# Kernel optimization log

Hardware: AMD Instinct MI355X
Metric: run time of the kernel (lower is better)

Reference implementation:

```python
import jax, jax.numpy as jnp
import numpy as np

NUM_HEADS = 8
BLOCK = 8      # block_size
HALO = 2       # kernel_size (halo width)


def _rel_to_abs(rel):
    # halo-style relative->absolute conversion
    # rel: [B, G, qh, qw, 2*p-1] -> [B, G, qh, qw, p]
    B, G, qh, qw, dim = rel.shape
    p = (dim + 1) // 2
    gap = p - qw
    flat = rel.reshape(B, G, qh, qw * dim)[:, :, :, qw - 1:-1]
    return flat.reshape(B, G, qh, qw, 2 * (p - 1))[:, :, :, :, gap:p + gap]


def _relative_logits(pos_q, pos_emb_h, pos_emb_w):
    # pos_q: [B, G, qb, qb, kd]; pos_emb_*: [kd, 2*p-1]
    rel_w = _rel_to_abs(jnp.einsum('bghwd,dr->bghwr', pos_q, pos_emb_w))  # [B,G,qb,qb,p] key-width
    q_t = pos_q.transpose(0, 1, 3, 2, 4)
    rel_h = _rel_to_abs(jnp.einsum('bgwhd,dr->bgwhr', q_t, pos_emb_h))
    rel_h = rel_h.transpose(0, 1, 3, 2, 4)  # [B,G,qb,qb,p] key-height
    return rel_h[..., :, None] + rel_w[..., None, :]  # [B,G,qb,qb,p,p]


def reference(x, w_q, w_kv, w_out, pos_emb_h, pos_emb_w):
    B, H, W, C = x.shape
    kd = C // NUM_HEADS                # per-head key dim
    kvk = BLOCK + 2 * HALO             # halo window size
    out_ch = w_out.shape[1]
    v_dim = out_ch // NUM_HEADS
    kv_per_head = (C + out_ch) // NUM_HEADS
    hh, ww = H // BLOCK, W // BLOCK
    scale = float(1.0 / np.sqrt(kd))

    # ---- query (1x1 conv == matmul), blockify ----
    q = (x @ w_q).reshape(B, hh, BLOCK, ww, BLOCK, NUM_HEADS, kd)
    q = q.transpose(0, 5, 1, 3, 2, 4, 6)  # [B,nh,hh,ww,qb,qb,kd]
    attn_q = q.reshape(B, NUM_HEADS, hh, ww, BLOCK * BLOCK, kd) * scale
    pos_q = q.reshape(B, NUM_HEADS * hh * ww, BLOCK, BLOCK, kd)

    # ---- key/value: 1x1 conv, halo pad, unfold into overlapping windows ----
    kv = jnp.pad(x @ w_kv, ((0, 0), (HALO, HALO), (HALO, HALO), (0, 0)))
    idx = np.arange(hh)[:, None] * BLOCK + np.arange(kvk)[None, :]  # [hh,kvk]
    idy = np.arange(ww)[:, None] * BLOCK + np.arange(kvk)[None, :]  # [ww,kvk]
    patches = kv[:, idx][:, :, :, idy]           # [B,hh,kvk,ww,kvk,kv_dim]
    patches = patches.transpose(0, 1, 3, 2, 4, 5)  # [B,hh,ww,kvk,kvk,kv_dim]
    kvh = patches.reshape(B, hh, ww, kvk, kvk, NUM_HEADS, kv_per_head)
    kvh = kvh.transpose(0, 5, 1, 2, 3, 4, 6).reshape(B, NUM_HEADS, hh, ww, kvk * kvk, kv_per_head)
    key, value = kvh[..., :kd], kvh[..., kd:]

    # ---- attention with relative position bias ----
    scores = jnp.einsum('bnhwqd,bnhwkd->bnhwqk', attn_q, key)
    pos = _relative_logits(pos_q, pos_emb_h, pos_emb_w)
    pos = pos.reshape(B, NUM_HEADS, hh, ww, BLOCK * BLOCK, kvk * kvk)
    attn = jax.nn.softmax(scores + pos, axis=-1)
    out = jnp.einsum('bnhwqk,bnhwkv->bnhwqv', attn, value)  # [B,nh,hh,ww,qb*qb,v_dim]

    # ---- de-blockify, output projection ----
    out = out.reshape(B, NUM_HEADS, hh, ww, BLOCK, BLOCK, v_dim)
    out = out.transpose(0, 2, 4, 3, 5, 1, 6).reshape(B, H, W, NUM_HEADS * v_dim)
    return out @ w_out


def setup_inputs() -> dict:
    key = jax.random.key(0)
    ks = jax.random.split(key, 6)
    B, H, W, C = 4, 128, 128, 256
    out_ch = 256
    kd = C // NUM_HEADS
    kvk = BLOCK + 2 * HALO
    std = kd ** -0.5
    return {
        'x': jax.random.normal(ks[0], (B, H, W, C), jnp.float32),
        'w_q': jax.random.normal(ks[1], (C, C), jnp.float32) * 0.02,
        'w_kv': jax.random.normal(ks[2], (C, C + out_ch), jnp.float32) * 0.02,
        'w_out': jax.random.normal(ks[3], (C, out_ch), jnp.float32) * 0.02,
        'pos_emb_h': jax.random.normal(ks[4], (kd, 2 * kvk - 1), jnp.float32) * std,
        'pos_emb_w': jax.random.normal(ks[5], (kd, 2 * kvk - 1), jnp.float32) * std,
    }
```

## Files before the change

kernel.cpp:

```cpp
#include <hip/hip_runtime.h>
#include <hip/hip_bf16.h>
#include <cstdint>


#define KVK 12
#define NKEYS 144
#define VT_S 160
#define PT_S 168
#define LOG2E 1.4426950408889634f

typedef unsigned int u32;
typedef unsigned long long u64;
typedef unsigned short u16;
typedef __attribute__((ext_vector_type(8))) __bf16 bf16x8;
typedef __attribute__((ext_vector_type(4))) float f32x4;

__device__ __forceinline__ u16 f2bf(float f) {
    u32 x = __float_as_uint(f);
    return (u16)((x + 0x7fffu + ((x >> 16) & 1u)) >> 16);
}
__device__ __forceinline__ u32 cvtpk(float lo, float hi) {
    u32 d;
    asm("v_cvt_pk_bf16_f32 %0, %1, %2" : "=v"(d) : "v"(lo), "v"(hi));
    return d;
}
__device__ __forceinline__ float max3f(float a, float b, float c) {
    float d;
    asm("v_max3_f32 %0, %1, %2, %3" : "=v"(d) : "v"(a), "v"(b), "v"(c));
    return d;
}
__device__ __forceinline__ float exp2a(float x) {
    float d;
    asm("v_exp_f32 %0, %1" : "=v"(d) : "v"(x));
    return d;
}
__device__ __forceinline__ void gload16(const void* g, void* l) {
    __builtin_amdgcn_global_load_lds(
        (const __attribute__((address_space(1))) void*)g,
        (__attribute__((address_space(3))) void*)l, 16, 0, 0);
}
__device__ __forceinline__ u32 pack2(float lo, float hi) {
    return (u32)f2bf(lo) | ((u32)f2bf(hi) << 16);
}

__global__ __launch_bounds__(256) void conv_prep(const float* __restrict__ x,
                                                 u16* __restrict__ xb,
                                                 const float* __restrict__ wq,
                                                 const float* __restrict__ wkv,
                                                 const float* __restrict__ wout,
                                                 u16* __restrict__ wT,
                                                 u16* __restrict__ woutT,
                                                 const float* __restrict__ emb_h,
                                                 const float* __restrict__ emb_w,
                                                 u16* __restrict__ embT) {
    int blk = blockIdx.x, t = threadIdx.x;
    if (blk < 8192) {
        int i = blk * 256 + t;
        const float4* p = reinterpret_cast<const float4*>(x) + (long)i * 2;
        float4 a = p[0], b = p[1];
        uint4 o;
        o.x = pack2(a.x, a.y); o.y = pack2(a.z, a.w);
        o.z = pack2(b.x, b.y); o.w = pack2(b.z, b.w);
        reinterpret_cast<uint4*>(xb)[i] = o;
        return;
    }
    blk -= 8192;
    if (blk < 256) {
        int idx = blk * 256 + t; int nn = idx >> 8, k = idx & 255;
        wT[idx] = f2bf(wq[(long)k * 256 + nn]);
    } else if (blk < 768) {
        int idx = (blk - 256) * 256 + t; int nn = idx >> 8, k = idx & 255;
        float v = wkv[(long)k * 512 + nn];
        if ((nn & 32) == 0) v *= 0.2550348642f;
        wT[65536 + idx] = f2bf(v);
    } else if (blk < 1024) {
        int idx = (blk - 768) * 256 + t; int nn = idx >> 8, k = idx & 255;
        woutT[idx] = f2bf(wout[(long)k * 256 + nn]);
    } else if (blk == 1024) {
        for (int i = t; i < 1024; i += 256) {
            int p = i >> 5, d = i & 31;
            embT[i] = (p < 23) ? f2bf(emb_h[d * 23 + p]) : 0;
        }
    } else {
        for (int i = t; i < 1024; i += 256) {
            int p = i >> 5, d = i & 31;
            embT[1024 + i] = (p < 23) ? f2bf(emb_w[d * 23 + p]) : 0;
        }
    }
}

__global__ __launch_bounds__(256) void gemm_qkv6(const u16* __restrict__ A,
                                                 const u16* __restrict__ WT,
                                                 u16* __restrict__ Qb,
                                                 u16* __restrict__ KVb) {
    __shared__ u16 As[8192];
    __shared__ u16 Bs[8192];
    const int t = threadIdx.x;
    const int bid = blockIdx.x;
    const int mIdx = (bid / 48) * 8 + (bid & 7);
    const int nt = (bid >> 3) % 6;
    const int w = t >> 6, lane = t & 63;
    const long m0 = (long)mIdx * 128;
    const long n0 = (long)nt * 128;
    const int wr = w >> 1, wc = w & 1;
    const int r = lane & 15, g = lane >> 4;

    f32x4 acc[4][4];
    #pragma unroll
    for (int i = 0; i < 4; ++i)
        #pragma unroll
        for (int j = 0; j < 4; ++j) acc[i][j] = (f32x4){0.f, 0.f, 0.f, 0.f};

    const u16* Ags[4];
    const u16* Bgs[4];
    #pragma unroll
    for (int cq = 0; cq < 4; ++cq) {
        int u = cq * 256 + w * 64 + lane;
        int panel = u >> 9, row = (u >> 2) & 127, col8 = (u & 3) * 8;
        Ags[cq] = A + (m0 + row) * 256 + panel * 32 + col8;
        Bgs[cq] = WT + (n0 + row) * 256 + panel * 32 + col8;
    }

    for (int k0 = 0; k0 < 256; k0 += 64) {
        #pragma unroll
        for (int cq = 0; cq < 4; ++cq) {
            gload16(Ags[cq] + k0, &As[cq * 2048 + w * 512]);
            gload16(Bgs[cq] + k0, &Bs[cq * 2048 + w * 512]);
        }
        __syncthreads();
        #pragma unroll
        for (int kk = 0; kk < 2; ++kk) {
            bf16x8 a[4], b[4];
            #pragma unroll
            for (int i = 0; i < 4; ++i)
                a[i] = *reinterpret_cast<const bf16x8*>(
                    &As[kk * 4096 + (wr * 64 + i * 16 + r) * 32 + g * 8]);
            #pragma unroll
            for (int j = 0; j < 4; ++j)
                b[j] = *reinterpret_cast<const bf16x8*>(
                    &Bs[kk * 4096 + (wc * 64 + j * 16 + r) * 32 + g * 8]);
            #pragma unroll
            for (int i = 0; i < 4; ++i)
                #pragma unroll
                for (int j = 0; j < 4; ++j)
                    acc[i][j] = __builtin_amdgcn_mfma_f32_16x16x32_bf16(b[j], a[i], acc[i][j], 0, 0, 0);
        }
        __syncthreads();
    }

    const bool isQ = (nt < 2);
    #pragma unroll
    for (int i = 0; i < 4; ++i) {
        long row = m0 + wr * 64 + i * 16 + r;
        #pragma unroll
        for (int j = 0; j < 4; ++j) {
            long colb = n0 + wc * 64 + j * 16 + g * 4;
            uint2 st;
            st.x = cvtpk(acc[i][j][0], acc[i][j][1]);
            st.y = cvtpk(acc[i][j][2], acc[i][j][3]);
            if (isQ) *reinterpret_cast<uint2*>(Qb + row * 256 + colb) = st;
            else     *reinterpret_cast<uint2*>(KVb + row * 512 + colb - 256) = st;
        }
    }
}

__global__ __launch_bounds__(256) void mfma_gemm(const u16* __restrict__ A,
                                                 const u16* __restrict__ BT,
                                                 float* __restrict__ C, int N) {
    __shared__ u16 As[8192];
    __shared__ u16 Bs[8192];
    const int t = threadIdx.x;
    const int bid = blockIdx.x;
    const int mIdx = (bid / 16) * 8 + (bid & 7);
    const int nt = (bid >> 3) & 1;
    const int w = t >> 6, lane = t & 63;
    const long m0 = (long)mIdx * 128;
    const long n0 = (long)nt * 128;
    const int wr = w >> 1, wc = w & 1;
    const int r = lane & 15, g = lane >> 4;

    f32x4 acc[4][4];
    #pragma unroll
    for (int i = 0; i < 4; ++i)
        #pragma unroll
        for (int j = 0; j < 4; ++j) acc[i][j] = (f32x4){0.f, 0.f, 0.f, 0.f};

    const u16* Ags[4];
    const u16* Bgs[4];
    #pragma unroll
    for (int cq = 0; cq < 4; ++cq) {
        int u = cq * 256 + w * 64 + lane;
        int panel = u >> 9, row = (u >> 2) & 127, col8 = (u & 3) * 8;
        Ags[cq] = A + (m0 + row) * 256 + panel * 32 + col8;
        Bgs[cq] = BT + (n0 + row) * 256 + panel * 32 + col8;
    }

    for (int k0 = 0; k0 < 256; k0 += 64) {
        #pragma unroll
        for (int cq = 0; cq < 4; ++cq) {
            gload16(Ags[cq] + k0, &As[cq * 2048 + w * 512]);
            gload16(Bgs[cq] + k0, &Bs[cq * 2048 + w * 512]);
        }
        __syncthreads();
        #pragma unroll
        for (int kk = 0; kk < 2; ++kk) {
            bf16x8 a[4], b[4];
            #pragma unroll
            for (int i = 0; i < 4; ++i)
                a[i] = *reinterpret_cast<const bf16x8*>(
                    &As[kk * 4096 + (wr * 64 + i * 16 + r) * 32 + g * 8]);
            #pragma unroll
            for (int j = 0; j < 4; ++j)
                b[j] = *reinterpret_cast<const bf16x8*>(
                    &Bs[kk * 4096 + (wc * 64 + j * 16 + r) * 32 + g * 8]);
            #pragma unroll
            for (int i = 0; i < 4; ++i)
                #pragma unroll
                for (int j = 0; j < 4; ++j)
                    acc[i][j] = __builtin_amdgcn_mfma_f32_16x16x32_bf16(b[j], a[i], acc[i][j], 0, 0, 0);
        }
        __syncthreads();
    }

    #pragma unroll
    for (int i = 0; i < 4; ++i) {
        long row = m0 + wr * 64 + i * 16 + r;
        #pragma unroll
        for (int j = 0; j < 4; ++j) {
            long colb = n0 + wc * 64 + j * 16 + g * 4;
            float4 st = make_float4(acc[i][j][0], acc[i][j][1], acc[i][j][2], acc[i][j][3]);
            *reinterpret_cast<float4*>(C + row * N + colb) = st;
        }
    }
}

#define UNITLOAD(U, VK, VV, KD, VB) {                                          \
    int kk_ = (U) >> 2, p_ = (U) & 3;                                          \
    int ky_ = (kk_ * 171) >> 11, kx_ = kk_ - 12 * ky_;                         \
    int gy_ = by * 8 + ky_ - 2, gx_ = bx * 8 + kx_ - 2;                        \
    if (((unsigned)gy_ < 128u) && ((unsigned)gx_ < 128u)) {                    \
        const u16* bp_ = KVb + (((long)b * 128 + gy_) * 128 + gx_) * 512 + n * 64 + p_ * 8; \
        VK = *reinterpret_cast<const uint4*>(bp_);                             \
        VV = *reinterpret_cast<const uint4*>(bp_ + 32);                        \
    }                                                                          \
    KD = kk_ * 64 + ((p_ * 8) ^ ((kk_ & 7) << 3));                             \
    VB = (p_ * 8) * VT_S + (kk_ ^ (p_ << 3));                                  \
}
#define VSCAT(VV, VB) {                                                        \
    u16 tmp_[8];                                                               \
    *reinterpret_cast<uint4*>(tmp_) = VV;                                      \
    _Pragma("unroll")                                                          \
    for (int i_ = 0; i_ < 8; ++i_) Vt[(VB) + i_ * VT_S] = tmp_[i_];            \
}

__global__ __launch_bounds__(256, 5) void attn_mfma(const u16* __restrict__ Qb,
                                                    const u16* __restrict__ KVb,
                                                    const u16* __restrict__ embT,
                                                    u16* __restrict__ Ob) {
    __shared__ __align__(16) char blob[22528];
    u16* Ks  = (u16*)blob;
    u16* Qe  = (u16*)(blob + 18432);
    u16* PT  = (u16*)blob;
    __shared__ u16 Vt[32 * VT_S];

    const int gblk = blockIdx.x;
    const int n = gblk & 7;
    const int bx = (gblk >> 3) & 15;
    const int by = (gblk >> 7) & 15;
    const int b = gblk >> 11;
    const int t = threadIdx.x;
    const int w = t >> 6, lane = t & 63;
    const int g = lane >> 4, r = lane & 15;

    const int q = w * 16 + r;
    const int qi = q >> 3, qj = q & 7;
    const long qrow = ((long)b * 128 + by * 8 + qi) * 128 + bx * 8 + qj;

    bf16x8 qa1 = *reinterpret_cast<const bf16x8*>(Qb + qrow * 256 + n * 32 + g * 8);
    bf16x8 ah0 = *reinterpret_cast<const bf16x8*>(embT + r * 32 + g * 8);
    bf16x8 ah1 = *reinterpret_cast<const bf16x8*>(embT + (16 + r) * 32 + g * 8);
    bf16x8 aw0 = *reinterpret_cast<const bf16x8*>(embT + 1024 + r * 32 + g * 8);
    bf16x8 aw1 = *reinterpret_cast<const bf16x8*>(embT + 1024 + (16 + r) * 32 + g * 8);

    uint4 z4 = make_uint4(0u, 0u, 0u, 0u);
    uint4 vK0 = z4, vV0 = z4, vK1 = z4, vV1 = z4, vK2 = z4, vV2 = z4;
    int kd0 = 0, vb0 = 0, kd1 = 0, vb1 = 0, kd2 = 0, vb2 = 0;
    UNITLOAD(t, vK0, vV0, kd0, vb0);
    UNITLOAD(t + 256, vK1, vV1, kd1, vb1);
    if (t < 64) UNITLOAD(t + 512, vK2, vV2, kd2, vb2);

    for (int u = t; u < 576; u += 256) {
        int kk = u >> 2, uu = u & 3;
        int ky = (kk * 171) >> 11;
        int kx = kk - 12 * ky;
        int hy = ky - 8 * uu;
        int hx = 12 + kx - 8 * uu;
        u64 lo = 0, hi = 0;
        if ((unsigned)hy < 4u) lo |= 0x3F80ULL << (hy * 16);
        else if ((unsigned)hy < 8u) hi |= 0x3F80ULL << ((hy - 4) * 16);
        if ((unsigned)hx < 4u) lo |= 0x3F80ULL << (hx * 16);
        else if ((unsigned)hx < 8u) hi |= 0x3F80ULL << ((hx - 4) * 16);
        int col = (32 + uu * 8) ^ ((kk & 7) << 3);
        u64* dst = reinterpret_cast<u64*>(&Ks[kk * 64 + col]);
        dst[0] = lo;
        dst[1] = hi;
    }
    if (t < 64) *reinterpret_cast<uint4*>(&Qe[t * 32 + 24]) = z4;
    if (t >= 224) {
        int d = t - 224;
        int sw = ((d >> 3) & 3) << 3;
        *reinterpret_cast<uint4*>(&Vt[d * VT_S + (144 ^ sw)]) = z4;
        *reinterpret_cast<uint4*>(&Vt[d * VT_S + (152 ^ sw)]) = z4;
    }

    *reinterpret_cast<uint4*>(&Ks[kd0]) = vK0;
    *reinterpret_cast<uint4*>(&Ks[kd1]) = vK1;
    if (t < 64) *reinterpret_cast<uint4*>(&Ks[kd2]) = vK2;

    {
        f32x4 z = (f32x4){0.f, 0.f, 0.f, 0.f};
        __builtin_amdgcn_s_setprio(1);
        f32x4 rh0 = __builtin_amdgcn_mfma_f32_16x16x32_bf16(ah0, qa1, z, 0, 0, 0);
        f32x4 rh1 = __builtin_amdgcn_mfma_f32_16x16x32_bf16(ah1, qa1, z, 0, 0, 0);
        f32x4 rw0 = __builtin_amdgcn_mfma_f32_16x16x32_bf16(aw0, qa1, z, 0, 0, 0);
        f32x4 rw1 = __builtin_amdgcn_mfma_f32_16x16x32_bf16(aw1, qa1, z, 0, 0, 0);
        __builtin_amdgcn_s_setprio(0);
        #pragma unroll
        for (int ti = 0; ti < 2; ++ti) {
            #pragma unroll
            for (int e = 0; e < 4; ++e) {
                int p = ti * 16 + g * 4 + e;
                float vh = (ti ? rh1[e] : rh0[e]) * LOG2E;
                float vw = (ti ? rw1[e] : rw0[e]) * LOG2E;
                int kyd = p + qi - 11;
                int kxd = p + qj - 11;
                if ((unsigned)kyd < 12u) Qe[q * 32 + kyd] = f2bf(vh);
                if ((unsigned)kxd < 12u) Qe[q * 32 + 12 + kxd] = f2bf(vw);
            }
        }
    }

    VSCAT(vV0, vb0);
    VSCAT(vV1, vb1);
    if (t < 64) VSCAT(vV2, vb2);

    __syncthreads();

    bf16x8 qa2 = *reinterpret_cast<const bf16x8*>(&Qe[q * 32 + g * 8]);
    f32x4 acc[9];
    __builtin_amdgcn_s_setprio(1);
    #pragma unroll
    for (int j = 0; j < 9; ++j) {
        int krow = j * 16 + r;
        int sw = (r & 7) << 3;
        bf16x8 kb0 = *reinterpret_cast<const bf16x8*>(&Ks[krow * 64 + ((g * 8) ^ sw)]);
        bf16x8 kb1 = *reinterpret_cast<const bf16x8*>(&Ks[krow * 64 + ((32 + g * 8) ^ sw)]);
        f32x4 z = (f32x4){0.f, 0.f, 0.f, 0.f};
        acc[j] = __builtin_amdgcn_mfma_f32_16x16x32_bf16(kb1, qa2,
                 __builtin_amdgcn_mfma_f32_16x16x32_bf16(kb0, qa1, z, 0, 0, 0), 0, 0, 0);
    }
    __builtin_amdgcn_s_setprio(0);

    float mx = max3f(acc[0][0], acc[0][1], acc[0][2]);
    mx = fmaxf(mx, acc[0][3]);
    #pragma unroll
    for (int j = 1; j < 9; ++j)
        mx = max3f(mx, max3f(acc[j][0], acc[j][1], acc[j][2]), acc[j][3]);
    mx = fmaxf(mx, __shfl_xor(mx, 16));
    mx = fmaxf(mx, __shfl_xor(mx, 32));
    float s0 = 0.f, s1 = 0.f, s2 = 0.f, s3 = 0.f;
    u32 pkA[9], pkB[9];
    #pragma unroll
    for (int j = 0; j < 9; ++j) {
        float e0 = exp2a(acc[j][0] - mx);
        float e1 = exp2a(acc[j][1] - mx);
        float e2 = exp2a(acc[j][2] - mx);
        float e3 = exp2a(acc[j][3] - mx);
        s0 += e0; s1 += e1; s2 += e2; s3 += e3;
        pkA[j] = cvtpk(e0, e1);
        pkB[j] = cvtpk(e2, e3);
    }
    float sum = (s0 + s1) + (s2 + s3);
    sum += __shfl_xor(sum, 16);
    sum += __shfl_xor(sum, 32);
    const float inv = __builtin_amdgcn_rcpf(sum);

    __syncthreads();

    {
        const int ptb = q * PT_S;
        #pragma unroll
        for (int j = 0; j < 9; ++j)
            *reinterpret_cast<uint2*>(&PT[ptb + 16 * j + 4 * g]) = make_uint2(pkA[j], pkB[j]);
        if (g == 0) {
            *reinterpret_cast<uint4*>(&PT[ptb + 144]) = make_uint4(0u, 0u, 0u, 0u);
            *reinterpret_cast<uint4*>(&PT[ptb + 152]) = make_uint4(0u, 0u, 0u, 0u);
        }
    }

    const int sw0 = (r >> 3) << 3;
    const int sw1 = (2 + (r >> 3)) << 3;
    f32x4 o0 = (f32x4){0.f, 0.f, 0.f, 0.f};
    f32x4 o1 = (f32x4){0.f, 0.f, 0.f, 0.f};
    __builtin_amdgcn_s_setprio(1);
    #pragma unroll
    for (int kk = 0; kk < 5; ++kk) {
        bf16x8 pb = *reinterpret_cast<const bf16x8*>(&PT[q * PT_S + kk * 32 + g * 8]);
        bf16x8 va0 = *reinterpret_cast<const bf16x8*>(&Vt[r * VT_S + ((kk * 32 + g * 8) ^ sw0)]);
        bf16x8 va1 = *reinterpret_cast<const bf16x8*>(&Vt[(16 + r) * VT_S + ((kk * 32 + g * 8) ^ sw1)]);
        o0 = __builtin_amdgcn_mfma_f32_16x16x32_bf16(va0, pb, o0, 0, 0, 0);
        o1 = __builtin_amdgcn_mfma_f32_16x16x32_bf16(va1, pb, o1, 0, 0, 0);
    }
    __builtin_amdgcn_s_setprio(0);
    {
        uint2 st0, st1;
        st0.x = cvtpk(o0[0] * inv, o0[1] * inv);
        st0.y = cvtpk(o0[2] * inv, o0[3] * inv);
        st1.x = cvtpk(o1[0] * inv, o1[1] * inv);
        st1.y = cvtpk(o1[2] * inv, o1[3] * inv);
        *reinterpret_cast<uint2*>(Ob + qrow * 256 + n * 32 + g * 4) = st0;
        *reinterpret_cast<uint2*>(Ob + qrow * 256 + n * 32 + 16 + g * 4) = st1;
    }
}

extern "C" void kernel_launch(void* const* d_in, const int* in_sizes, int n_in,
                              void* d_out, int out_size, void* d_ws, size_t ws_size,
                              hipStream_t stream) {
    const float* x     = (const float*)d_in[0];
    const float* w_q   = (const float*)d_in[1];
    const float* w_kv  = (const float*)d_in[2];
    const float* w_out = (const float*)d_in[3];
    const float* emb_h = (const float*)d_in[4];
    const float* emb_w = (const float*)d_in[5];

    u16* xb = (u16*)d_out;
    u16* Qb = (u16*)((char*)d_out + (size_t)33554432);
    char* ws = (char*)d_ws;
    u16* KVb   = (u16*)(ws);
    u16* Ob    = (u16*)(ws + (size_t)67108864);
    u16* wT    = (u16*)(ws + (size_t)100663296);
    u16* woutT = (u16*)(ws + (size_t)100663296 + 393216);
    u16* embT  = (u16*)(ws + (size_t)100663296 + 524288);

    dim3 blk(256);
    conv_prep<<<dim3(9218), blk, 0, stream>>>(x, xb, w_q, w_kv, w_out, wT, woutT,
                                              emb_h, emb_w, embT);
    gemm_qkv6<<<dim3(3072), blk, 0, stream>>>(xb, wT, Qb, KVb);
    attn_mfma<<<dim3(8192), blk, 0, stream>>>(Qb, KVb, embT, Ob);
    mfma_gemm<<<dim3(1024), blk, 0, stream>>>(Ob, woutT, (float*)d_out, 256);
}
```

Measured before the change: 131.7 us.

## Double-buffer LDS tiles in projection GEMMs to overlap loads with MFMA

Both projection GEMM kernels now split K into eight 32-wide steps and ping-pong between two LDS halves. The next step's global-to-LDS copies are issued before the MFMAs on the current buffer run, with one barrier per step instead of two. The goal is to hide global load latency behind compute. It depends on gload16 being asynchronous and on a single barrier per step being enough to guard the buffer being overwritten.

```diff
diff --git a/kernel.cpp b/kernel.cpp
--- a/kernel.cpp
+++ b/kernel.cpp
@@ -111,41 +111,47 @@
         #pragma unroll
         for (int j = 0; j < 4; ++j) acc[i][j] = (f32x4){0.f, 0.f, 0.f, 0.f};
 
-    const u16* Ags[4];
-    const u16* Bgs[4];
-    #pragma unroll
-    for (int cq = 0; cq < 4; ++cq) {
-        int u = cq * 256 + w * 64 + lane;
-        int panel = u >> 9, row = (u >> 2) & 127, col8 = (u & 3) * 8;
-        Ags[cq] = A + (m0 + row) * 256 + panel * 32 + col8;
-        Bgs[cq] = WT + (n0 + row) * 256 + panel * 32 + col8;
-    }
-
-    for (int k0 = 0; k0 < 256; k0 += 64) {
-        #pragma unroll
-        for (int cq = 0; cq < 4; ++cq) {
-            gload16(Ags[cq] + k0, &As[cq * 2048 + w * 512]);
-            gload16(Bgs[cq] + k0, &Bs[cq * 2048 + w * 512]);
-        }
+    const int u0 = w * 128 + lane;
+    const int row0 = u0 >> 2, cs0 = (u0 & 3) * 8;
+    const int u1 = u0 + 64;
+    const int row1 = u1 >> 2, cs1 = (u1 & 3) * 8;
+    const u16* Ag0 = A + (m0 + row0) * 256 + cs0;
+    const u16* Ag1 = A + (m0 + row1) * 256 + cs1;
+    const u16* Bg0 = WT + (n0 + row0) * 256 + cs0;
+    const u16* Bg1 = WT + (n0 + row1) * 256 + cs1;
+    const int wb = w * 1024;
+
+    gload16(Ag0, &As[wb]);
+    gload16(Ag1, &As[wb + 512]);
+    gload16(Bg0, &Bs[wb]);
+    gload16(Bg1, &Bs[wb + 512]);
+
+    #pragma unroll
+    for (int k = 0; k < 8; ++k) {
         __syncthreads();
-        #pragma unroll
-        for (int kk = 0; kk < 2; ++kk) {
-            bf16x8 a[4], b[4];
-            #pragma unroll
-            for (int i = 0; i < 4; ++i)
-                a[i] = *reinterpret_cast<const bf16x8*>(
-                    &As[kk * 4096 + (wr * 64 + i * 16 + r) * 32 + g * 8]);
+        if (k < 7) {
+            const int nb = ((k + 1) & 1) * 4096;
+            const int ko = (k + 1) * 32;
+            gload16(Ag0 + ko, &As[nb + wb]);
+            gload16(Ag1 + ko, &As[nb + wb + 512]);
+            gload16(Bg0 + ko, &Bs[nb + wb]);
+            gload16(Bg1 + ko, &Bs[nb + wb + 512]);
+        }
+        const int cb = (k & 1) * 4096;
+        bf16x8 a[4], b[4];
+        #pragma unroll
+        for (int i = 0; i < 4; ++i)
+            a[i] = *reinterpret_cast<const bf16x8*>(
+                &As[cb + (wr * 64 + i * 16 + r) * 32 + g * 8]);
+        #pragma unroll
+        for (int j = 0; j < 4; ++j)
+            b[j] = *reinterpret_cast<const bf16x8*>(
+                &Bs[cb + (wc * 64 + j * 16 + r) * 32 + g * 8]);
+        #pragma unroll
+        for (int i = 0; i < 4; ++i)
             #pragma unroll
             for (int j = 0; j < 4; ++j)
-                b[j] = *reinterpret_cast<const bf16x8*>(
-                    &Bs[kk * 4096 + (wc * 64 + j * 16 + r) * 32 + g * 8]);
-            #pragma unroll
-            for (int i = 0; i < 4; ++i)
-                #pragma unroll
-                for (int j = 0; j < 4; ++j)
-                    acc[i][j] = __builtin_amdgcn_mfma_f32_16x16x32_bf16(b[j], a[i], acc[i][j], 0, 0, 0);
-        }
-        __syncthreads();
+                acc[i][j] = __builtin_amdgcn_mfma_f32_16x16x32_bf16(b[j], a[i], acc[i][j], 0, 0, 0);
     }
 
     const bool isQ = (nt < 2);
@@ -185,41 +191,47 @@
         #pragma unroll
         for (int j = 0; j < 4; ++j) acc[i][j] = (f32x4){0.f, 0.f, 0.f, 0.f};
 
-    const u16* Ags[4];
-    const u16* Bgs[4];
-    #pragma unroll
-    for (int cq = 0; cq < 4; ++cq) {
-        int u = cq * 256 + w * 64 + lane;
-        int panel = u >> 9, row = (u >> 2) & 127, col8 = (u & 3) * 8;
-        Ags[cq] = A + (m0 + row) * 256 + panel * 32 + col8;
-        Bgs[cq] = BT + (n0 + row) * 256 + panel * 32 + col8;
-    }
-
-    for (int k0 = 0; k0 < 256; k0 += 64) {
-        #pragma unroll
-        for (int cq = 0; cq < 4; ++cq) {
-            gload16(Ags[cq] + k0, &As[cq * 2048 + w * 512]);
-            gload16(Bgs[cq] + k0, &Bs[cq * 2048 + w * 512]);
-        }
+    const int u0 = w * 128 + lane;
+    const int row0 = u0 >> 2, cs0 = (u0 & 3) * 8;
+    const int u1 = u0 + 64;
+    const int row1 = u1 >> 2, cs1 = (u1 & 3) * 8;
+    const u16* Ag0 = A + (m0 + row0) * 256 + cs0;
+    const u16* Ag1 = A + (m0 + row1) * 256 + cs1;
+    const u16* Bg0 = BT + (n0 + row0) * 256 + cs0;
+    const u16* Bg1 = BT + (n0 + row1) * 256 + cs1;
+    const int wb = w * 1024;
+
+    gload16(Ag0, &As[wb]);
+    gload16(Ag1, &As[wb + 512]);
+    gload16(Bg0, &Bs[wb]);
+    gload16(Bg1, &Bs[wb + 512]);
+
+    #pragma unroll
+    for (int k = 0; k < 8; ++k) {
         __syncthreads();
-        #pragma unroll
-        for (int kk = 0; kk < 2; ++kk) {
-            bf16x8 a[4], b[4];
-            #pragma unroll
-            for (int i = 0; i < 4; ++i)
-                a[i] = *reinterpret_cast<const bf16x8*>(
-                    &As[kk * 4096 + (wr * 64 + i * 16 + r) * 32 + g * 8]);
+        if (k < 7) {
+            const int nb = ((k + 1) & 1) * 4096;
+            const int ko = (k + 1) * 32;
+            gload16(Ag0 + ko, &As[nb + wb]);
+            gload16(Ag1 + ko, &As[nb + wb + 512]);
+            gload16(Bg0 + ko, &Bs[nb + wb]);
+            gload16(Bg1 + ko, &Bs[nb + wb + 512]);
+        }
+        const int cb = (k & 1) * 4096;
+        bf16x8 a[4], b[4];
+        #pragma unroll
+        for (int i = 0; i < 4; ++i)
+            a[i] = *reinterpret_cast<const bf16x8*>(
+                &As[cb + (wr * 64 + i * 16 + r) * 32 + g * 8]);
+        #pragma unroll
+        for (int j = 0; j < 4; ++j)
+            b[j] = *reinterpret_cast<const bf16x8*>(
+                &Bs[cb + (wc * 64 + j * 16 + r) * 32 + g * 8]);
+        #pragma unroll
+        for (int i = 0; i < 4; ++i)
             #pragma unroll
             for (int j = 0; j < 4; ++j)
-                b[j] = *reinterpret_cast<const bf16x8*>(
-                    &Bs[kk * 4096 + (wc * 64 + j * 16 + r) * 32 + g * 8]);
-            #pragma unroll
-            for (int i = 0; i < 4; ++i)
-                #pragma unroll
-                for (int j = 0; j < 4; ++j)
-                    acc[i][j] = __builtin_amdgcn_mfma_f32_16x16x32_bf16(b[j], a[i], acc[i][j], 0, 0, 0);
-        }
-        __syncthreads();
+                acc[i][j] = __builtin_amdgcn_mfma_f32_16x16x32_bf16(b[j], a[i], acc[i][j], 0, 0, 0);
     }
 
     #pragma unroll
```

After: 137.1 us. 4.1% more time.
